# Kernel optimization log

Measured on AMD Instinct MI355X. Metric: run time of the kernel, lower is better.

Reference implementation:

```python
import jax, jax.numpy as jnp
import numpy as np

B, T, F, H = 128, 256, 64, 512

def glorot(key, shape):
    fan_in, fan_out = shape[0], shape[1]
    lim = jnp.sqrt(6.0 / (fan_in + fan_out))
    return jax.random.uniform(key, shape, jnp.float32, -lim, lim)

def setup_inputs() -> dict:
    key = jax.random.key(0)
    ks = jax.random.split(key, 8)
    x = jax.random.normal(ks[0], (B, T, F), jnp.float32)
    W1 = glorot(ks[1], (F, H)); b1 = jnp.zeros((H,), jnp.float32)
    Wx1 = glorot(ks[2], (H, 4 * H)); Wh1 = glorot(ks[3], (H, 4 * H))
    blstm1 = jnp.concatenate([jnp.zeros((H,)), jnp.ones((H,)), jnp.zeros((2 * H,))]).astype(jnp.float32)  # keras unit_forget_bias
    Wx2 = glorot(ks[4], (H, 4 * H)); Wh2 = glorot(ks[5], (H, 4 * H))
    blstm2 = jnp.concatenate([jnp.zeros((H,)), jnp.ones((H,)), jnp.zeros((2 * H,))]).astype(jnp.float32)
    gamma = jnp.ones((H,), jnp.float32); beta = jnp.zeros((H,), jnp.float32)
    W2 = glorot(ks[6], (H, H // 2)); b2 = jnp.zeros((H // 2,), jnp.float32)
    W3 = glorot(ks[7], (H // 2, 1)); b3 = jnp.zeros((1,), jnp.float32)
    return dict(x=x, W1=W1, b1=b1, Wx1=Wx1, Wh1=Wh1, blstm1=blstm1,
                Wx2=Wx2, Wh2=Wh2, blstm2=blstm2, gamma=gamma, beta=beta,
                W2=W2, b2=b2, W3=W3, b3=b3)

def lstm(x, Wx, Wh, b):
    # x: [B, T, Din] -> sequence of hidden states [B, T, H] and last h [B, H]
    h_dim = Wh.shape[0]
    xg = jnp.einsum('btd,dg->btg', x, Wx) + b  # precompute input contributions [B,T,4H]
    def step(carry, xt):
        h, c = carry
        g = xt + h @ Wh
        i, f, cb, o = jnp.split(g, 4, axis=-1)
        i = jax.nn.sigmoid(i); f = jax.nn.sigmoid(f); o = jax.nn.sigmoid(o)
        c = f * c + i * jnp.tanh(cb)
        h = o * jnp.tanh(c)
        return (h, c), h
    init = (jnp.zeros((x.shape[0], h_dim), x.dtype), jnp.zeros((x.shape[0], h_dim), x.dtype))
    (h_last, _), hs = jax.lax.scan(step, init, jnp.swapaxes(xg, 0, 1))
    return jnp.swapaxes(hs, 0, 1), h_last

def reference(x, W1, b1, Wx1, Wh1, blstm1, Wx2, Wh2, blstm2, gamma, beta, W2, b2, W3, b3):
    h = x @ W1 + b1                                  # dense1 [B,T,H]
    # spectral_norm lambda: L2-normalize last axis, scale by sqrt(H)
    norm = jnp.linalg.norm(h, axis=-1, keepdims=True)
    h = h / jnp.maximum(norm, 1e-12) * jnp.sqrt(jnp.float32(h.shape[-1]))
    seq, _ = lstm(h, Wx1, Wh1, blstm1)               # lstm1 return_sequences
    _, h2 = lstm(seq, Wx2, Wh2, blstm2)              # lstm2 last output [B,H]
    mu = jnp.mean(h2, axis=-1, keepdims=True)
    var = jnp.mean((h2 - mu) ** 2, axis=-1, keepdims=True)
    h2 = (h2 - mu) * jax.lax.rsqrt(var + 1e-3) * gamma + beta  # keras LayerNorm eps=1e-3
    h3 = jax.nn.relu(h2 @ W2 + b2)
    return h3 @ W3 + b3                               # [B,1]
```

## Files before the change

### kernel.cpp

```cpp
#include <hip/hip_runtime.h>
#include <hip/hip_bf16.h>
#include <math.h>

#define B_ 128
#define T_ 256
#define F_ 64
#define H_ 512
#define G4_ 2048

#define XB0_OFF 0
#define XB1_OFF 32768
#define HB_OFF  65536
#define GLD_OFF 98304
#define SMEM_TOTAL 115712

typedef __attribute__((ext_vector_type(8))) short bf16x8;
typedef __attribute__((ext_vector_type(4))) float f32x4;

__device__ __forceinline__ void coh_store_u32(unsigned* p, unsigned v) {
  __hip_atomic_store(p, v, __ATOMIC_RELAXED, __HIP_MEMORY_SCOPE_AGENT);
}
__device__ __forceinline__ unsigned coh_load_u32(const unsigned* p) {
  return __hip_atomic_load(p, __ATOMIC_RELAXED, __HIP_MEMORY_SCOPE_AGENT);
}
__device__ __forceinline__ void rawbar() { __builtin_amdgcn_s_barrier(); }

__device__ __forceinline__ void async_ld16(const void* g, void* l) {
  __builtin_amdgcn_global_load_lds(
      (const __attribute__((address_space(1))) void*)g,
      (__attribute__((address_space(3))) void*)l, 16, 0, 0);
}
__device__ __forceinline__ void async_ld16c(const void* g, void* l) {
  __builtin_amdgcn_global_load_lds(
      (const __attribute__((address_space(1))) void*)g,
      (__attribute__((address_space(3))) void*)l, 16, 0, 17);
}

__device__ __forceinline__ float fsig(float x) {
  float e = __builtin_amdgcn_exp2f(-1.44269504089f * x);
  return __builtin_amdgcn_rcpf(1.f + e);
}
__device__ __forceinline__ float ftanh(float x) {
  float ax = __builtin_fabsf(x);
  float e = __builtin_amdgcn_exp2f(-2.88539008177f * ax);
  float r = (1.f - e) * __builtin_amdgcn_rcpf(1.f + e);
  return __builtin_copysignf(r, x);
}

__global__ __launch_bounds__(256) void transpose_cast_k(
    const float* __restrict__ s0, const float* __restrict__ s1,
    const float* __restrict__ s2, const float* __restrict__ s3,
    __hip_bfloat16* __restrict__ dst)
{
  __shared__ float lds[64][65];
  const float* src = (blockIdx.z == 0) ? s0 : (blockIdx.z == 1) ? s1 : (blockIdx.z == 2) ? s2 : s3;
  __hip_bfloat16* d = dst + (size_t)blockIdx.z * (G4_ * H_);
  int n0 = blockIdx.x * 64, k0 = blockIdx.y * 64;
  int tx = threadIdx.x & 63, ty = threadIdx.x >> 6;
#pragma unroll
  for (int r = 0; r < 16; r++) { int k = r * 4 + ty; lds[k][tx] = src[(size_t)(k0 + k) * G4_ + n0 + tx]; }
  __syncthreads();
#pragma unroll
  for (int r = 0; r < 16; r++) { int n = r * 4 + ty; d[(size_t)(n0 + n) * H_ + k0 + tx] = __float2bfloat16(lds[tx][n]); }
}

__global__ void prep_misc_k(const float* __restrict__ w1, __hip_bfloat16* __restrict__ w1b,
                            float* __restrict__ zbase, int nzero)
{
  int i = blockIdx.x * blockDim.x + threadIdx.x;
  int stride = gridDim.x * blockDim.x;
  for (int k = i; k < F_ * H_; k += stride) w1b[k] = __float2bfloat16(w1[k]);
  for (int k = i; k < nzero; k += stride) zbase[k] = 0.f;
}

__global__ __launch_bounds__(512) void dense1_k(
    const float* __restrict__ x, const __hip_bfloat16* __restrict__ w1b,
    const float* __restrict__ b1, __hip_bfloat16* __restrict__ h0)
{
  __shared__ float red[8];
  int j = threadIdx.x;
  int wave = j >> 6, lane = j & 63;
  float wcol[64];
#pragma unroll
  for (int k = 0; k < 64; k++) wcol[k] = __bfloat162float(w1b[k * H_ + j]);
  float bj = b1[j];
  for (int r = 0; r < 32; r++) {
    int row = blockIdx.x * 32 + r;
    const float* xr = x + (size_t)row * F_;
    float acc = bj;
#pragma unroll
    for (int k = 0; k < 64; k++) acc += xr[k] * wcol[k];
    float ss = acc * acc;
#pragma unroll
    for (int o = 32; o; o >>= 1) ss += __shfl_down(ss, o);
    if (lane == 0) red[wave] = ss;
    __syncthreads();
    float tot = red[0] + red[1] + red[2] + red[3] + red[4] + red[5] + red[6] + red[7];
    float sc = sqrtf(512.f) / fmaxf(sqrtf(tot), 1e-12f);
    h0[(size_t)row * H_ + j] = __float2bfloat16(acc * sc);
    __syncthreads();
  }
}

#define RUN_CHAIN(BASEPTR, W0, W1, A0, A1)                                    \
  {                                                                           \
    const char* _cb = (const char*)(BASEPTR);                                 \
    _Pragma("unroll")                                                         \
    for (int kc = 0; kc < 8; kc++) {                                          \
      bf16x8 _av = *(const bf16x8*)(_cb + ((mh * 16 + kh * 8 + kc) << 10) + (lane << 4)); \
      A0 = __builtin_amdgcn_mfma_f32_16x16x32_bf16(_av, W0[kc], A0, 0, 0, 0); \
      A1 = __builtin_amdgcn_mfma_f32_16x16x32_bf16(_av, W1[kc], A1, 0, 0, 0); \
    }                                                                         \
  }

__global__ __launch_bounds__(512, 2) void lstm_fused_k(
    const __hip_bfloat16* __restrict__ h0,
    __hip_bfloat16* __restrict__ seq,
    const __hip_bfloat16* __restrict__ wh1, const __hip_bfloat16* __restrict__ wx1,
    const float* __restrict__ bl1,
    const __hip_bfloat16* __restrict__ wh2, const __hip_bfloat16* __restrict__ wx2,
    const float* __restrict__ bl2,
    __hip_bfloat16* __restrict__ h1A, __hip_bfloat16* __restrict__ h1B,
    __hip_bfloat16* __restrict__ h2A, __hip_bfloat16* __restrict__ h2B,
    float* __restrict__ h2f,
    unsigned* flags)
{
  extern __shared__ char smem[];
  float* gld = (float*)(smem + GLD_OFF);
  const int tid = threadIdx.x;
  const int wave = tid >> 6;
  const int lane = tid & 63;
  const int lr = lane & 15;
  const int lk = lane >> 4;
  const int bid = blockIdx.x;
  const int grp = bid >> 7;
  const int lid = bid & 127;
  const int bb = lid & 3;
  const int bu = lid >> 2;
  const int m0 = bb * 32;
  const int u0 = bu * 16;

  const int kh = wave >> 2;
  const int mh = (wave >> 1) & 1;
  const int gp = wave & 1;

  const __hip_bfloat16* Wht = grp ? wh2 : wh1;
  const __hip_bfloat16* Wxt = grp ? wx2 : wx1;
  const __hip_bfloat16* xsrc = grp ? (const __hip_bfloat16*)seq : h0;
  const float* bias = grp ? bl2 : bl1;
  __hip_bfloat16* hgA = grp ? h2A : h1A;
  __hip_bfloat16* hgB = grp ? h2B : h1B;
  unsigned* cown  = flags + (((grp << 2) | bb) << 8);
  unsigned* cprod = flags + (bb << 8);

  bf16x8 wh_0[8], wh_1[8], wx_0[8], wx_1[8];
  {
    const size_t c0 = (size_t)((gp * 2 + 0) * 512 + u0 + lr) * H_ + kh * 256 + lk * 8;
    const size_t c1 = (size_t)((gp * 2 + 1) * 512 + u0 + lr) * H_ + kh * 256 + lk * 8;
#pragma unroll
    for (int kc = 0; kc < 8; kc++) {
      wh_0[kc] = *(const bf16x8*)(Wht + c0 + kc * 32);
      wh_1[kc] = *(const bf16x8*)(Wht + c1 + kc * 32);
      wx_0[kc] = *(const bf16x8*)(Wxt + c0 + kc * 32);
      wx_1[kc] = *(const bf16x8*)(Wxt + c1 + kc * 32);
    }
#pragma unroll
    for (int kc = 0; kc < 8; kc++) {
      asm volatile("" : "+v"(wh_0[kc]), "+v"(wh_1[kc]), "+v"(wx_0[kc]), "+v"(wx_1[kc]));
    }
  }

  const int m_e = tid >> 3, up_e = tid & 7;
  float br0[2], br1[2], br2[2], br3[2];
  float2 creg = {0.f, 0.f};
  if (tid < 256) {
#pragma unroll
    for (int c = 0; c < 2; c++) {
      br0[c] = bias[0 * 512 + u0 + 2 * up_e + c];
      br1[c] = bias[1 * 512 + u0 + 2 * up_e + c];
      br2[c] = bias[2 * 512 + u0 + 2 * up_e + c];
      br3[c] = bias[3 * 512 + u0 + 2 * up_e + c];
    }
  }

  char* xb0 = smem + XB0_OFF;
  char* xb1 = smem + XB1_OFF;

  auto issue_x = [&](int t, char* xb) {
#pragma unroll
    for (int j = 0; j < 4; j++) {
      const int c = wave * 4 + j;
      const __hip_bfloat16* g = xsrc +
          ((size_t)(m0 + (c >> 4) * 16 + lr) * T_ + t) * H_ + (c & 15) * 32 + lk * 8;
      if (grp) async_ld16c(g, xb + c * 1024);
      else     async_ld16(g, xb + c * 1024);
    }
  };
  auto issue_h = [&](int u) {
#pragma unroll
    for (int j = 0; j < 4; j++) {
      const int c = wave * 4 + j;
      const int row = m0 + (c >> 4) * 16 + lr;
      const __hip_bfloat16* g;
      if (grp) {
        const __hip_bfloat16* hsrc = ((u - 1) & 1) ? hgB : hgA;
        g = hsrc + (size_t)row * H_ + (c & 15) * 32 + lk * 8;
      } else {
        g = seq + ((size_t)row * T_ + (u - 1)) * H_ + (c & 15) * 32 + lk * 8;
      }
      async_ld16c(g, smem + HB_OFF + c * 1024);
    }
  };
  auto wait2 = [&](unsigned t0, bool need1, unsigned t1) {
    while (true) {
      unsigned v0 = coh_load_u32(cown);
      if (v0 >= t0) {
        if (!need1) break;
        unsigned v1 = coh_load_u32(cprod);
        if (v1 >= t1) break;
      }
      __builtin_amdgcn_s_sleep(1);
    }
  };
  auto spinA = [&](int u) {
    const bool need1 = (grp == 1) && (u <= T_ - 3);
    wait2((unsigned)(32 * u), need1, (unsigned)(32 * (u + 3)));
  };
  auto publish = [&]() {
    if (tid == 0) atomicAdd(cown, 1u);
  };
  auto write_gld = [&](f32x4 s0, f32x4 s1) {
    float* d0 = gld + ((kh * 4 + gp * 2 + 0) * 32 + mh * 16 + lk * 4) * 17 + lr;
    float* d1 = gld + ((kh * 4 + gp * 2 + 1) * 32 + mh * 16 + lk * 4) * 17 + lr;
#pragma unroll
    for (int r = 0; r < 4; r++) { d0[r * 17] = s0[r]; d1[r * 17] = s1[r]; }
  };
  auto elem = [&](int u, __hip_bfloat16* hout) {
    if (tid < 256) {
      float gv0[2], gv1[2], gv2[2], gv3[2];
#pragma unroll
      for (int c = 0; c < 2; c++) {
        const int o = m_e * 17 + 2 * up_e + c;
        gv0[c] = gld[(0 * 32) * 17 + o] + gld[(4 * 32) * 17 + o] + br0[c];
        gv1[c] = gld[(1 * 32) * 17 + o] + gld[(5 * 32) * 17 + o] + br1[c];
        gv2[c] = gld[(2 * 32) * 17 + o] + gld[(6 * 32) * 17 + o] + br2[c];
        gv3[c] = gld[(3 * 32) * 17 + o] + gld[(7 * 32) * 17 + o] + br3[c];
      }
      float i0 = fsig(gv0[0]), i1 = fsig(gv0[1]);
      float f0 = fsig(gv1[0]), f1 = fsig(gv1[1]);
      float cb0 = ftanh(gv2[0]), cb1 = ftanh(gv2[1]);
      float o0 = fsig(gv3[0]), o1 = fsig(gv3[1]);
      float cn0 = f0 * creg.x + i0 * cb0;
      float cn1 = f1 * creg.y + i1 * cb1;
      creg.x = cn0; creg.y = cn1;
      float hv0 = o0 * ftanh(cn0), hv1 = o1 * ftanh(cn1);
      union { __hip_bfloat16 h[2]; unsigned u32; } pk;
      pk.h[0] = __float2bfloat16(hv0);
      pk.h[1] = __float2bfloat16(hv1);
      const int row = m0 + m_e, col = u0 + 2 * up_e;
      if (grp == 0) {
        coh_store_u32((unsigned*)seq + (((size_t)row * T_ + u) * H_ + col) / 2, pk.u32);
      } else {
        coh_store_u32((unsigned*)hout + ((size_t)row * H_ + col) / 2, pk.u32);
        if (u == T_ - 1) {
          float2 hv = {hv0, hv1};
          *(float2*)(h2f + (size_t)row * H_ + col) = hv;
        }
      }
    }
  };

  f32x4 axc0 = {0.f,0.f,0.f,0.f}, axc1 = {0.f,0.f,0.f,0.f};
  f32x4 axn0, axn1, ah0, ah1;

  if (grp) wait2(0u, true, 96u);
  issue_x(0, xb0);
  issue_x(1, xb1);
  asm volatile("s_waitcnt vmcnt(0)" ::: "memory");
  rawbar();
  __builtin_amdgcn_sched_barrier(0);
  RUN_CHAIN(xb0, wx_0, wx_1, axc0, axc1);
  write_gld(axc0, axc1);
  asm volatile("s_waitcnt lgkmcnt(0)" ::: "memory");
  rawbar();
  __builtin_amdgcn_sched_barrier(0);
  elem(0, hgA);
  issue_x(2, xb0);
  asm volatile("s_waitcnt vmcnt(4)" ::: "memory");
  publish();
  asm volatile("s_waitcnt vmcnt(0)" ::: "memory");
  rawbar();
  __builtin_amdgcn_sched_barrier(0);
  axc0 = (f32x4){0.f,0.f,0.f,0.f}; axc1 = (f32x4){0.f,0.f,0.f,0.f};
  RUN_CHAIN(xb1, wx_0, wx_1, axc0, axc1);

  for (int u = 1; u < T_; u++) {
    __hip_bfloat16* hout = (u & 1) ? hgB : hgA;
    const bool pf = (u <= T_ - 3);

    spinA(u);
    issue_h(u);
    if (u < T_ - 1) {
      axn0 = (f32x4){0.f,0.f,0.f,0.f}; axn1 = (f32x4){0.f,0.f,0.f,0.f};
      char* xb = ((u + 1) & 1) ? xb1 : xb0;
      RUN_CHAIN(xb, wx_0, wx_1, axn0, axn1);
    }
    asm volatile("s_waitcnt vmcnt(0)" ::: "memory");
    rawbar();
    __builtin_amdgcn_sched_barrier(0);
    ah0 = (f32x4){0.f,0.f,0.f,0.f}; ah1 = (f32x4){0.f,0.f,0.f,0.f};
    RUN_CHAIN(smem + HB_OFF, wh_0, wh_1, ah0, ah1);
    write_gld(axc0 + ah0, axc1 + ah1);
    asm volatile("s_waitcnt lgkmcnt(0)" ::: "memory");
    rawbar();
    __builtin_amdgcn_sched_barrier(0);
    elem(u, hout);
    if (pf) {
      issue_x(u + 2, (u & 1) ? xb1 : xb0);
      asm volatile("s_waitcnt vmcnt(4)" ::: "memory");
      publish();
      asm volatile("s_waitcnt vmcnt(0)" ::: "memory");
    } else {
      asm volatile("s_waitcnt vmcnt(0)" ::: "memory");
      publish();
    }
    rawbar();
    axc0 = axn0; axc1 = axn1;
  }
}

__global__ __launch_bounds__(256) void final_k(
    const float* __restrict__ h2, const float* __restrict__ gamma, const float* __restrict__ beta,
    const float* __restrict__ W2, const float* __restrict__ b2,
    const float* __restrict__ W3, const float* __restrict__ b3, float* __restrict__ out)
{
  __shared__ float y[512];
  __shared__ float redS[4], redQ[4], redP[4];
  int b = blockIdx.x, tid = threadIdx.x;
  int wave = tid >> 6, lane = tid & 63;
  float v0 = h2[b * H_ + tid], v1 = h2[b * H_ + 256 + tid];
  float s = v0 + v1, q = v0 * v0 + v1 * v1;
#pragma unroll
  for (int o = 32; o; o >>= 1) { s += __shfl_down(s, o); q += __shfl_down(q, o); }
  if (lane == 0) { redS[wave] = s; redQ[wave] = q; }
  __syncthreads();
  float tot = redS[0] + redS[1] + redS[2] + redS[3];
  float totq = redQ[0] + redQ[1] + redQ[2] + redQ[3];
  float mu = tot * (1.f / 512.f);
  float var = totq * (1.f / 512.f) - mu * mu;
  float rs = rsqrtf(var + 1e-3f);
  y[tid]       = (v0 - mu) * rs * gamma[tid] + beta[tid];
  y[tid + 256] = (v1 - mu) * rs * gamma[tid + 256] + beta[tid + 256];
  __syncthreads();
  float acc = b2[tid];
  for (int k = 0; k < 512; k++) acc += y[k] * W2[k * 256 + tid];
  float pv = fmaxf(acc, 0.f) * W3[tid];
#pragma unroll
  for (int o = 32; o; o >>= 1) pv += __shfl_down(pv, o);
  if (lane == 0) redP[wave] = pv;
  __syncthreads();
  if (tid == 0) out[b] = redP[0] + redP[1] + redP[2] + redP[3] + b3[0];
}

extern "C" void kernel_launch(void* const* d_in, const int* in_sizes, int n_in,
                              void* d_out, int out_size, void* d_ws, size_t ws_size,
                              hipStream_t stream)
{
  (void)in_sizes; (void)n_in; (void)out_size; (void)ws_size;
  const float* x    = (const float*)d_in[0];
  const float* W1   = (const float*)d_in[1];
  const float* b1   = (const float*)d_in[2];
  const float* Wx1  = (const float*)d_in[3];
  const float* Wh1  = (const float*)d_in[4];
  const float* bl1  = (const float*)d_in[5];
  const float* Wx2  = (const float*)d_in[6];
  const float* Wh2  = (const float*)d_in[7];
  const float* bl2  = (const float*)d_in[8];
  const float* gam  = (const float*)d_in[9];
  const float* bet  = (const float*)d_in[10];
  const float* W2   = (const float*)d_in[11];
  const float* b2   = (const float*)d_in[12];
  const float* W3   = (const float*)d_in[13];
  const float* b3   = (const float*)d_in[14];

  char* p = (char*)d_ws;
  const size_t MB = 1024 * 1024;
  __hip_bfloat16* wx1t = (__hip_bfloat16*)(p + 0 * MB);
  __hip_bfloat16* wh1t = (__hip_bfloat16*)(p + 2 * MB);
  __hip_bfloat16* wx2t = (__hip_bfloat16*)(p + 4 * MB);
  __hip_bfloat16* wh2t = (__hip_bfloat16*)(p + 6 * MB);
  __hip_bfloat16* w1b  = (__hip_bfloat16*)(p + 8 * MB);
  __hip_bfloat16* h0   = (__hip_bfloat16*)(p + 9 * MB);
  __hip_bfloat16* seq  = (__hip_bfloat16*)(p + 41 * MB);
  char* st = p + 73 * MB;
  __hip_bfloat16* h1A = (__hip_bfloat16*)st;
  __hip_bfloat16* h1B = h1A + B_ * H_;
  __hip_bfloat16* h2A = h1B + B_ * H_;
  __hip_bfloat16* h2B = h2A + B_ * H_;
  float* h2f = (float*)(st + 512 * 1024);
  unsigned* flags = (unsigned*)(st + 512 * 1024 + 256 * 1024);
  int nzero = (int)((512 * 1024 + 256 * 1024 + 16384) / 4);

  transpose_cast_k<<<dim3(32, 8, 4), 256, 0, stream>>>(Wx1, Wh1, Wx2, Wh2, wx1t);
  prep_misc_k<<<256, 256, 0, stream>>>(W1, w1b, (float*)st, nzero);
  dense1_k<<<1024, 512, 0, stream>>>(x, w1b, b1, h0);

  void* args[] = { (void*)&h0, (void*)&seq,
                   (void*)&wh1t, (void*)&wx1t, (void*)&bl1,
                   (void*)&wh2t, (void*)&wx2t, (void*)&bl2,
                   (void*)&h1A, (void*)&h1B, (void*)&h2A, (void*)&h2B,
                   (void*)&h2f, (void*)&flags };
  hipLaunchCooperativeKernel((void*)lstm_fused_k, dim3(256), dim3(512), args,
                             SMEM_TOTAL, stream);

  final_k<<<128, 256, 0, stream>>>(h2f, gam, bet, W2, b2, W3, b3, (float*)d_out);
}
```

Measured before the change: 1.124 ms.

## Remove per-step block barrier by having each wave load its own h span

Each wave now issues async loads for exactly the h chunks its own MFMA chain consumes, so the block-wide barrier between the h load and the recurrent matmul is dropped. The input-projection partials go to a separate LDS gate buffer, written early, and the elementwise stage sums the x and h buffers. The spin-wait now busy-polls before it starts sleeping, to react faster to producer flags. This costs extra LDS and more LDS reads in the elementwise stage, and relies on each wave's chunk mapping matching the RUN_CHAIN consumption pattern.

```diff
diff --git a/kernel.cpp b/kernel.cpp
--- a/kernel.cpp
+++ b/kernel.cpp
@@ -11,8 +11,9 @@
 #define XB0_OFF 0
 #define XB1_OFF 32768
 #define HB_OFF  65536
-#define GLD_OFF 98304
-#define SMEM_TOTAL 115712
+#define GLDX_OFF 98304
+#define GLDH_OFF 115712
+#define SMEM_TOTAL 133120
 
 typedef __attribute__((ext_vector_type(8))) short bf16x8;
 typedef __attribute__((ext_vector_type(4))) float f32x4;
@@ -126,7 +127,8 @@
     unsigned* flags)
 {
   extern __shared__ char smem[];
-  float* gld = (float*)(smem + GLD_OFF);
+  float* gldx = (float*)(smem + GLDX_OFF);
+  float* gldh = (float*)(smem + GLDH_OFF);
   const int tid = threadIdx.x;
   const int wave = tid >> 6;
   const int lane = tid & 63;
@@ -196,10 +198,11 @@
       else     async_ld16(g, xb + c * 1024);
     }
   };
-  auto issue_h = [&](int u) {
-#pragma unroll
-    for (int j = 0; j < 4; j++) {
-      const int c = wave * 4 + j;
+  auto issue_h_span = [&](int u) {
+    const int s = mh * 16 + kh * 8;
+#pragma unroll
+    for (int j = 0; j < 8; j++) {
+      const int c = s + j;
       const int row = m0 + (c >> 4) * 16 + lr;
       const __hip_bfloat16* g;
       if (grp) {
@@ -212,6 +215,7 @@
     }
   };
   auto wait2 = [&](unsigned t0, bool need1, unsigned t1) {
+    int n = 0;
     while (true) {
       unsigned v0 = coh_load_u32(cown);
       if (v0 >= t0) {
@@ -219,7 +223,7 @@
         unsigned v1 = coh_load_u32(cprod);
         if (v1 >= t1) break;
       }
-      __builtin_amdgcn_s_sleep(1);
+      if (++n > 48) __builtin_amdgcn_s_sleep(2);
     }
   };
   auto spinA = [&](int u) {
@@ -229,22 +233,28 @@
   auto publish = [&]() {
     if (tid == 0) atomicAdd(cown, 1u);
   };
-  auto write_gld = [&](f32x4 s0, f32x4 s1) {
-    float* d0 = gld + ((kh * 4 + gp * 2 + 0) * 32 + mh * 16 + lk * 4) * 17 + lr;
-    float* d1 = gld + ((kh * 4 + gp * 2 + 1) * 32 + mh * 16 + lk * 4) * 17 + lr;
+  auto write_gld = [&](float* g, f32x4 s0, f32x4 s1) {
+    float* d0 = g + ((kh * 4 + gp * 2 + 0) * 32 + mh * 16 + lk * 4) * 17 + lr;
+    float* d1 = g + ((kh * 4 + gp * 2 + 1) * 32 + mh * 16 + lk * 4) * 17 + lr;
 #pragma unroll
     for (int r = 0; r < 4; r++) { d0[r * 17] = s0[r]; d1[r * 17] = s1[r]; }
   };
-  auto elem = [&](int u, __hip_bfloat16* hout) {
+  auto elem = [&](int u, __hip_bfloat16* hout, bool with_h) {
     if (tid < 256) {
       float gv0[2], gv1[2], gv2[2], gv3[2];
 #pragma unroll
       for (int c = 0; c < 2; c++) {
         const int o = m_e * 17 + 2 * up_e + c;
-        gv0[c] = gld[(0 * 32) * 17 + o] + gld[(4 * 32) * 17 + o] + br0[c];
-        gv1[c] = gld[(1 * 32) * 17 + o] + gld[(5 * 32) * 17 + o] + br1[c];
-        gv2[c] = gld[(2 * 32) * 17 + o] + gld[(6 * 32) * 17 + o] + br2[c];
-        gv3[c] = gld[(3 * 32) * 17 + o] + gld[(7 * 32) * 17 + o] + br3[c];
+        gv0[c] = gldx[(0 * 32) * 17 + o] + gldx[(4 * 32) * 17 + o] + br0[c];
+        gv1[c] = gldx[(1 * 32) * 17 + o] + gldx[(5 * 32) * 17 + o] + br1[c];
+        gv2[c] = gldx[(2 * 32) * 17 + o] + gldx[(6 * 32) * 17 + o] + br2[c];
+        gv3[c] = gldx[(3 * 32) * 17 + o] + gldx[(7 * 32) * 17 + o] + br3[c];
+        if (with_h) {
+          gv0[c] += gldh[(0 * 32) * 17 + o] + gldh[(4 * 32) * 17 + o];
+          gv1[c] += gldh[(1 * 32) * 17 + o] + gldh[(5 * 32) * 17 + o];
+          gv2[c] += gldh[(2 * 32) * 17 + o] + gldh[(6 * 32) * 17 + o];
+          gv3[c] += gldh[(3 * 32) * 17 + o] + gldh[(7 * 32) * 17 + o];
+        }
       }
       float i0 = fsig(gv0[0]), i1 = fsig(gv0[1]);
       float f0 = fsig(gv1[0]), f1 = fsig(gv1[1]);
@@ -280,11 +290,11 @@
   rawbar();
   __builtin_amdgcn_sched_barrier(0);
   RUN_CHAIN(xb0, wx_0, wx_1, axc0, axc1);
-  write_gld(axc0, axc1);
+  write_gld(gldx, axc0, axc1);
   asm volatile("s_waitcnt lgkmcnt(0)" ::: "memory");
   rawbar();
   __builtin_amdgcn_sched_barrier(0);
-  elem(0, hgA);
+  elem(0, hgA, false);
   issue_x(2, xb0);
   asm volatile("s_waitcnt vmcnt(4)" ::: "memory");
   publish();
@@ -299,22 +309,21 @@
     const bool pf = (u <= T_ - 3);
 
     spinA(u);
-    issue_h(u);
+    issue_h_span(u);
+    write_gld(gldx, axc0, axc1);
     if (u < T_ - 1) {
       axn0 = (f32x4){0.f,0.f,0.f,0.f}; axn1 = (f32x4){0.f,0.f,0.f,0.f};
       char* xb = ((u + 1) & 1) ? xb1 : xb0;
       RUN_CHAIN(xb, wx_0, wx_1, axn0, axn1);
     }
     asm volatile("s_waitcnt vmcnt(0)" ::: "memory");
-    rawbar();
-    __builtin_amdgcn_sched_barrier(0);
     ah0 = (f32x4){0.f,0.f,0.f,0.f}; ah1 = (f32x4){0.f,0.f,0.f,0.f};
     RUN_CHAIN(smem + HB_OFF, wh_0, wh_1, ah0, ah1);
-    write_gld(axc0 + ah0, axc1 + ah1);
+    write_gld(gldh, ah0, ah1);
     asm volatile("s_waitcnt lgkmcnt(0)" ::: "memory");
     rawbar();
     __builtin_amdgcn_sched_barrier(0);
-    elem(u, hout);
+    elem(u, hout, true);
     if (pf) {
       issue_x(u + 2, (u & 1) ? xb1 : xb0);
       asm volatile("s_waitcnt vmcnt(4)" ::: "memory");
@@ -325,6 +334,7 @@
       publish();
     }
     rawbar();
+    __builtin_amdgcn_sched_barrier(0);
     axc0 = axn0; axc1 = axn1;
   }
 }
```

After: 1.326 ms. 18.0% more time.
